# Performance work log

Hardware: AMD Instinct MI355X
Metric: run time of the kernel (lower is better)

The kernel has to match this reference:

```python
import jax, jax.numpy as jnp
import numpy as np

B, H, W, C = 1, 64, 64, 256
NH = 8
K = 7


def setup_inputs() -> dict:
    key = jax.random.key(0)
    ks = jax.random.split(key, 6)
    x = jax.random.normal(ks[0], (B, H, W, C), dtype=jnp.float32)
    # torch nn.Linear weights are [out, in]
    qkv_w = jax.random.normal(ks[1], (3 * C, C), dtype=jnp.float32) * 0.02
    qkv_b = jnp.zeros((3 * C,), dtype=jnp.float32)
    proj_w = jax.random.normal(ks[2], (C, C), dtype=jnp.float32) * 0.02
    proj_b = jnp.zeros((C,), dtype=jnp.float32)
    # relative position bias table: [num_heads, 2K-1, 2K-1]
    rpb = jax.random.normal(ks[3], (NH, 2 * K - 1, 2 * K - 1), dtype=jnp.float32) * 0.02
    return {"x": x, "qkv_w": qkv_w, "qkv_b": qkv_b, "proj_w": proj_w,
            "proj_b": proj_b, "rpb": rpb}


def _neighbor_idx(n, k):
    # clamped window starts (NATTEN semantics): each query sees exactly k neighbors
    start = jnp.clip(jnp.arange(n) - k // 2, 0, n - k)  # [n]
    return start[:, None] + jnp.arange(k)[None, :]       # [n, k]


def reference(x, qkv_w, qkv_b, proj_w, proj_b, rpb):
    b, h, w, c = x.shape
    nh = rpb.shape[0]
    k = (rpb.shape[1] + 1) // 2
    hd = c // nh
    scale = hd ** -0.5

    qkv = x @ qkv_w.T + qkv_b                              # [b,h,w,3c]
    qkv = qkv.reshape(b, h, w, 3, nh, hd)
    qkv = jnp.transpose(qkv, (3, 0, 4, 1, 2, 5))           # [3,b,nh,h,w,hd]
    q, kk, v = qkv[0], qkv[1], qkv[2]

    ni = _neighbor_idx(h, k)                               # [h,k]
    nj = _neighbor_idx(w, k)                               # [w,k]

    # gather neighborhood keys/values: [b,nh,h,k,w,k,hd]
    k_nb = kk[:, :, ni][:, :, :, :, nj]
    v_nb = v[:, :, ni][:, :, :, :, nj]

    # attention logits over the k x k window
    attn = jnp.einsum('bnijd,bniajcd->bnijac', q * scale, k_nb)  # [b,nh,h,w,k,k]

    # relative position bias: index = (neighbor - query) + (k-1)
    bi = ni - jnp.arange(h)[:, None] + (k - 1)             # [h,k]
    bj = nj - jnp.arange(w)[:, None] + (k - 1)             # [w,k]
    bias = rpb[:, bi][:, :, :, bj]                         # [nh,h,k,w,k]
    attn = attn + jnp.transpose(bias, (0, 1, 3, 2, 4))[None]

    attn = jax.nn.softmax(attn.reshape(b, nh, h, w, k * k), axis=-1)
    attn = attn.reshape(b, nh, h, w, k, k)

    out = jnp.einsum('bnijac,bniajcd->bnijd', attn, v_nb)  # [b,nh,h,w,hd]
    out = jnp.transpose(out, (0, 2, 3, 1, 4)).reshape(b, h, w, c)
    out = out @ proj_w.T + proj_b
    return out
```

## Files before the change

### kernel.cpp

```cpp
#include <hip/hip_runtime.h>
#include <math.h>

#define HH 64
#define WW 64
#define CC 256
#define NHEAD 8
#define HD 32
#define KW 7
#define NPIX (HH * WW)

#define KR 40
#define VTS 232

typedef _Float16 half2v __attribute__((ext_vector_type(2)));
typedef _Float16 half8v __attribute__((ext_vector_type(8)));
typedef __fp16 fp16x2 __attribute__((ext_vector_type(2)));
typedef float float4v __attribute__((ext_vector_type(4)));

__device__ __forceinline__ unsigned pkrtz(float lo, float hi) {
  union { fp16x2 h; unsigned u; } c;
  c.h = __builtin_amdgcn_cvt_pkrtz(lo, hi);
  return c.u;
}
__device__ __forceinline__ ushort f2h(float f) {
  union { _Float16 h; ushort u; } c;
  c.h = (_Float16)f;
  return c.u;
}

template <int N, int BM, int BN, bool ABF, bool OB>
__global__ __launch_bounds__(256) void gemm5h(
    const void* __restrict__ Ap, const float* __restrict__ Bw,
    const float* __restrict__ bias, void* __restrict__ Cd) {
  constexpr int SEGA = BM / 32;
  constexpr int SEGB = BN / 32;
  constexpr int MF = BM / 32;
  constexpr int NF = BN / 32;

  __shared__ ushort As[2][BM * 64];
  __shared__ ushort Bs[2][BN * 64];

  const int t = threadIdx.x;
  const int lane = t & 63;
  const int wave = t >> 6;
  const int bm = blockIdx.x * BM;
  const int bn = blockIdx.y * BN;

  const float*  Aw = (const float*)Ap;
  const ushort* Ab = (const ushort*)Ap;

  float fA[2][SEGA][8];
  float fB[2][SEGB][8];
  uint4 wA[2][SEGA];

#define LOADA(c, s)                                                            \
  {                                                                            \
    _Pragma("unroll") for (int sa = 0; sa < SEGA; ++sa) {                      \
      const int seg = sa * 256 + t;                                            \
      const int row = seg >> 3;                                                \
      const int q8 = seg & 7;                                                  \
      if (ABF) {                                                               \
        wA[s][sa] =                                                            \
            *(const uint4*)(Ab + (size_t)(bm + row) * 256 + (c) * 64 + q8 * 8);\
      } else {                                                                 \
        const float* p_ = Aw + (size_t)(bm + row) * 256 + (c) * 64 + q8 * 8;   \
        *(float4*)&fA[s][sa][0] = *(const float4*)(p_);                        \
        *(float4*)&fA[s][sa][4] = *(const float4*)(p_ + 4);                    \
      }                                                                        \
    }                                                                          \
  }

#define LOADB(c, s)                                                            \
  {                                                                            \
    _Pragma("unroll") for (int sb = 0; sb < SEGB; ++sb) {                      \
      const int seg = sb * 256 + t;                                            \
      const int row = seg >> 3;                                                \
      const int q8 = seg & 7;                                                  \
      const float* p_ = Bw + (size_t)(bn + row) * 256 + (c) * 64 + q8 * 8;     \
      *(float4*)&fB[s][sb][0] = *(const float4*)(p_);                          \
      *(float4*)&fB[s][sb][4] = *(const float4*)(p_ + 4);                      \
    }                                                                          \
  }

#define WRITEC(b, s)                                                           \
  {                                                                            \
    _Pragma("unroll") for (int sa = 0; sa < SEGA; ++sa) {                      \
      const int seg = sa * 256 + t;                                            \
      const int row = seg >> 3;                                                \
      const int q8 = seg & 7;                                                  \
      const int lin = row * 128 + q8 * 16;                                     \
      const int sw = (row & 7) << 4;                                           \
      uint4 w_;                                                                \
      if (ABF) {                                                               \
        w_ = wA[s][sa];                                                        \
      } else {                                                                 \
        w_.x = pkrtz(fA[s][sa][0], fA[s][sa][1]);                              \
        w_.y = pkrtz(fA[s][sa][2], fA[s][sa][3]);                              \
        w_.z = pkrtz(fA[s][sa][4], fA[s][sa][5]);                              \
        w_.w = pkrtz(fA[s][sa][6], fA[s][sa][7]);                              \
      }                                                                        \
      *(uint4*)((char*)As[b] + (lin ^ sw)) = w_;                               \
    }                                                                          \
    _Pragma("unroll") for (int sb = 0; sb < SEGB; ++sb) {                      \
      const int seg = sb * 256 + t;                                            \
      const int row = seg >> 3;                                                \
      const int q8 = seg & 7;                                                  \
      const int lin = row * 128 + q8 * 16;                                     \
      const int sw = (row & 7) << 4;                                           \
      uint4 w_;                                                                \
      w_.x = pkrtz(fB[s][sb][0], fB[s][sb][1]);                                \
      w_.y = pkrtz(fB[s][sb][2], fB[s][sb][3]);                                \
      w_.z = pkrtz(fB[s][sb][4], fB[s][sb][5]);                                \
      w_.w = pkrtz(fB[s][sb][6], fB[s][sb][7]);                                \
      *(uint4*)((char*)Bs[b] + (lin ^ sw)) = w_;                               \
    }                                                                          \
  }

  const int wr = (wave >> 1) * (BM / 2);
  const int wc = (wave & 1) * (BN / 2);
  const int lrow = lane & 15;
  const int lkb = (lane >> 4) * 16;

  float4v acc[MF][NF];
#pragma unroll
  for (int mf = 0; mf < MF; ++mf)
#pragma unroll
    for (int nf = 0; nf < NF; ++nf) acc[mf][nf] = (float4v){0.f, 0.f, 0.f, 0.f};

  LOADA(0, 0); LOADB(0, 0);
  WRITEC(0, 0);
  LOADA(1, 1); LOADB(1, 1);
  __syncthreads();

#pragma unroll
  for (int c = 0; c < 4; ++c) {
    if (c < 3) WRITEC((c + 1) & 1, (c + 1) & 1);
    if (c < 2) { LOADA(c + 2, c & 1); LOADB(c + 2, c & 1); }
    const char* Al = (const char*)As[c & 1];
    const char* Bl = (const char*)Bs[c & 1];
#pragma unroll
    for (int ks = 0; ks < 2; ++ks) {
      half8v af[MF], bfr[NF];
#pragma unroll
      for (int mf = 0; mf < MF; ++mf) {
        const int row = wr + mf * 16 + lrow;
        const int ad = row * 128 + ks * 64 + lkb;
        af[mf] = *(const half8v*)(Al + (ad ^ ((row & 7) << 4)));
      }
#pragma unroll
      for (int nf = 0; nf < NF; ++nf) {
        const int row = wc + nf * 16 + lrow;
        const int bd = row * 128 + ks * 64 + lkb;
        bfr[nf] = *(const half8v*)(Bl + (bd ^ ((row & 7) << 4)));
      }
#pragma unroll
      for (int mf = 0; mf < MF; ++mf)
#pragma unroll
        for (int nf = 0; nf < NF; ++nf)
          acc[mf][nf] = __builtin_amdgcn_mfma_f32_16x16x32_f16(
              af[mf], bfr[nf], acc[mf][nf], 0, 0, 0);
    }
    if (c < 3) __syncthreads();
  }
#undef LOADA
#undef LOADB
#undef WRITEC

#pragma unroll
  for (int mf = 0; mf < MF; ++mf) {
#pragma unroll
    for (int nf = 0; nf < NF; ++nf) {
      const int n = bn + wc + nf * 16 + lrow;
      const float bv = bias[n];
      const int m0 = bm + wr + mf * 16 + (lane >> 4) * 4;
      if (OB) {
        ushort* C = (ushort*)Cd;
#pragma unroll
        for (int rr = 0; rr < 4; ++rr)
          C[(size_t)(m0 + rr) * N + n] = f2h(acc[mf][nf][rr] + bv);
      } else {
        float* C = (float*)Cd;
#pragma unroll
        for (int rr = 0; rr < 4; ++rr)
          C[(size_t)(m0 + rr) * N + n] = acc[mf][nf][rr] + bv;
      }
    }
  }
}

__global__ __launch_bounds__(256) void natten7(
    const ushort* __restrict__ qkv, const float* __restrict__ rpb,
    ushort* __restrict__ aout) {
  __shared__ ushort Ks[224 * KR];
  __shared__ ushort Vt[32 * VTS];
  __shared__ float Rs[169];

  const int head = blockIdx.y;
  const int tile = blockIdx.x;
  const int i0 = (tile >> 3) * 8, j0 = (tile & 7) * 8;
  const int hs = min(max(i0 - 3, 0), HH - 14);
  const int ws = min(max(j0 - 3, 0), WW - 14);
  const int t = threadIdx.x;
  const int l = t & 63;
  const int wv = t >> 6;

  if (t < 169) Rs[t] = rpb[head * 169 + t];

  if (t < 112) {
    const int ent2 = t >> 2;
    const int hr = ent2 >> 1, hc = 14 + (ent2 & 1);
    const uint4 z = {0u, 0u, 0u, 0u};
    *(uint4*)(Ks + (hr * 16 + hc) * KR + (t & 3) * 8) = z;
  }
#pragma unroll
  for (int it = 0; it < 2; ++it) {
    const int task = it * 256 + t;
    const int d = task >> 4, hr = task & 15;
    if (hr < 14) *(unsigned*)(Vt + d * VTS + hr * 16 + 14) = 0u;
  }

#pragma unroll
  for (int s = 0; s < 4; ++s) {
    if (t < 196) {
      const int hr = (t * 2341) >> 15;
      const int hc = t - hr * 14;
      const int g = (hs + hr) * WW + (ws + hc);
      const int col = hr * 16 + hc;
      const uint4 kv = *(const uint4*)(qkv + (size_t)g * 768 + 256 + head * HD + s * 8);
      *(uint4*)(Ks + col * KR + s * 8) = kv;
      const uint4 vv = *(const uint4*)(qkv + (size_t)g * 768 + 512 + head * HD + s * 8);
      const int d0 = s * 8;
      Vt[(d0 + 0) * VTS + col] = (ushort)(vv.x);
      Vt[(d0 + 1) * VTS + col] = (ushort)(vv.x >> 16);
      Vt[(d0 + 2) * VTS + col] = (ushort)(vv.y);
      Vt[(d0 + 3) * VTS + col] = (ushort)(vv.y >> 16);
      Vt[(d0 + 4) * VTS + col] = (ushort)(vv.z);
      Vt[(d0 + 5) * VTS + col] = (ushort)(vv.z >> 16);
      Vt[(d0 + 6) * VTS + col] = (ushort)(vv.w);
      Vt[(d0 + 7) * VTS + col] = (ushort)(vv.w >> 16);
    }
  }
  __syncthreads();

  const int strip_i0 = i0 + wv * 2;
  const int lg = l >> 4;
  const int l15 = l & 15;

  const int pi = strip_i0 + (l15 >> 3);
  const int pj = j0 + (l15 & 7);
  const int si = min(max(pi - 3, 0), HH - KW);
  const int sj = min(max(pj - 3, 0), WW - KW);
  const int si_min = min(max(strip_i0 - 3, 0), HH - KW);
  const int slab0 = min(si_min - hs, 6);

  const half8v qf = *(const half8v*)(qkv + (size_t)(pi * WW + pj) * 768 +
                                     head * HD + lg * 8);

  float4v s8[8];
  const float4v zz = {0.f, 0.f, 0.f, 0.f};
#pragma unroll
  for (int g = 0; g < 8; ++g) {
    const int ent = (slab0 + g) * 16 + l15;
    const half8v kf = *(const half8v*)(Ks + ent * KR + lg * 8);
    s8[g] = __builtin_amdgcn_mfma_f32_16x16x32_f16(kf, qf, zz, 0, 0, 0);
  }

  const int lr0 = si - hs;
  const int lc0 = sj - ws;
  const int abase = slab0 - lr0;
  const int rowb = ((si - pi + 6) + abase) * 13 + (sj - pj + 6) - lc0;
  const float scale = 0.17677669529663687f;

  float e8[8][4];
  float ssum = 0.f;
#pragma unroll
  for (int g = 0; g < 8; ++g) {
    const int a = abase + g;
    const bool va = (unsigned)a < 7u;
    const int idxg = min(max(rowb + g * 13, 0), 153);
#pragma unroll
    for (int r = 0; r < 4; ++r) {
      const int hc = lg * 4 + r;
      const bool vc = (unsigned)(hc - lc0) < 7u;
      const float ev = __expf(fmaf(s8[g][r], scale, Rs[idxg + hc]));
      const float em = (va && vc) ? ev : 0.f;
      e8[g][r] = em;
      ssum += em;
    }
  }
  ssum += __shfl_xor(ssum, 16);
  ssum += __shfl_xor(ssum, 32);
  const float inv = 1.f / ssum;

  unsigned Wp[8][2];
#pragma unroll
  for (int g = 0; g < 8; ++g) {
    Wp[g][0] = pkrtz(e8[g][0] * inv, e8[g][1] * inv);
    Wp[g][1] = pkrtz(e8[g][2] * inv, e8[g][3] * inv);
  }

  float4v o[2] = {zz, zz};
#pragma unroll
  for (int ks = 0; ks < 4; ++ks) {
    unsigned F[4];
#pragma unroll
    for (int f = 0; f < 4; ++f) {
      const int src = l15 + (((lg & 1) * 2 + (f >> 1)) << 4);
      const unsigned va = __shfl(Wp[2 * ks][f & 1], src);
      const unsigned vb = __shfl(Wp[2 * ks + 1][f & 1], src);
      F[f] = (lg >> 1) ? vb : va;
    }
    union { unsigned u[4]; half8v h; } pf;
    pf.u[0] = F[0]; pf.u[1] = F[1]; pf.u[2] = F[2]; pf.u[3] = F[3];
#pragma unroll
    for (int nf = 0; nf < 2; ++nf) {
      const int dim = l15 + nf * 16;
      const half8v vf = *(const half8v*)(Vt + dim * VTS + slab0 * 16 +
                                         ks * 32 + lg * 8);
      o[nf] = __builtin_amdgcn_mfma_f32_16x16x32_f16(pf.h, vf, o[nf], 0, 0, 0);
    }
  }

#pragma unroll
  for (int r = 0; r < 4; ++r) {
    const int pxo = lg * 4 + r;
    const int oi = strip_i0 + (pxo >> 3);
    const int oj = j0 + (pxo & 7);
    ushort* op = aout + (size_t)(oi * WW + oj) * CC + head * HD + l15;
    op[0]  = f2h(o[0][r]);
    op[16] = f2h(o[1][r]);
  }
}

extern "C" void kernel_launch(void* const* d_in, const int* in_sizes, int n_in,
                              void* d_out, int out_size, void* d_ws, size_t ws_size,
                              hipStream_t stream) {
  const float* x      = (const float*)d_in[0];
  const float* qkv_w  = (const float*)d_in[1];
  const float* qkv_b  = (const float*)d_in[2];
  const float* proj_w = (const float*)d_in[3];
  const float* proj_b = (const float*)d_in[4];
  const float* rpb    = (const float*)d_in[5];
  float* out = (float*)d_out;

  ushort* qkvh  = (ushort*)d_ws;
  ushort* aouth = qkvh + 3145728;

  gemm5h<768, 32, 64, false, true><<<dim3(128, 12), 256, 0, stream>>>(
      x, qkv_w, qkv_b, qkvh);

  natten7<<<dim3(64, NHEAD), 256, 0, stream>>>(qkvh, rpb, aouth);

  gemm5h<256, 32, 32, true, false><<<dim3(128, 8), 256, 0, stream>>>(
      aouth, proj_w, proj_b, out);
}
```

Before: 25.40 us.

## Fuse output projection GEMM into neighborhood attention kernel via last-block counters

Merges the projection GEMM into the attention kernel. Each block bumps per-tile atomic counters after writing its head's output. The last of the 8 head blocks to finish a 4-row half-tile then runs the 32x256 projection for it, reusing the attention shared memory. This drops one kernel launch and the gap between kernels. In exchange, the projection work lands on only a few tail blocks, and the counters are never reset, relying on modulo-8 wraparound across calls.

```diff
diff --git a/kernel.cpp b/kernel.cpp
--- a/kernel.cpp
+++ b/kernel.cpp
@@ -7,15 +7,16 @@
 #define NHEAD 8
 #define HD 32
 #define KW 7
-#define NPIX (HH * WW)
 
 #define KR 40
 #define VTS 232
 
-typedef _Float16 half2v __attribute__((ext_vector_type(2)));
 typedef _Float16 half8v __attribute__((ext_vector_type(8)));
 typedef __fp16 fp16x2 __attribute__((ext_vector_type(2)));
 typedef float float4v __attribute__((ext_vector_type(4)));
+
+struct PadCnt { unsigned v; unsigned pad[15]; };
+__device__ PadCnt half_cnt[128];
 
 __device__ __forceinline__ unsigned pkrtz(float lo, float hi) {
   union { fp16x2 h; unsigned u; } c;
@@ -188,19 +189,138 @@
   }
 }
 
-__global__ __launch_bounds__(256) void natten7(
+__device__ __forceinline__ void gemm2_half(
+    char* smem, const ushort* __restrict__ A, const float* __restrict__ Bw,
+    const float* __restrict__ bias, float* __restrict__ Cd,
+    int pr0, int j0, int bn, int t) {
+  constexpr int ABUF = 32 * 128;
+  constexpr int BBUF = 64 * 128;
+
+  char* As0 = smem;
+  char* Bs0 = smem + 2 * ABUF;
+
+  const int lane = t & 63;
+  const int wave = t >> 6;
+
+  uint4 wA[2];
+  float fB[2][2][8];
+
+#define LOADA2(c, s)                                                           \
+  {                                                                            \
+    const int row = t >> 3;                                                    \
+    const int q8 = t & 7;                                                      \
+    const int pix = (pr0 + (row >> 3)) * 64 + j0 + (row & 7);                  \
+    wA[s] = *(const uint4*)(A + (size_t)pix * 256 + (c) * 64 + q8 * 8);        \
+  }
+
+#define LOADB2(c, s)                                                           \
+  {                                                                            \
+    _Pragma("unroll") for (int sb = 0; sb < 2; ++sb) {                         \
+      const int seg = sb * 256 + t;                                            \
+      const int row = seg >> 3;                                                \
+      const int q8 = seg & 7;                                                  \
+      const float* p_ = Bw + (size_t)(bn + row) * 256 + (c) * 64 + q8 * 8;     \
+      *(float4*)&fB[s][sb][0] = *(const float4*)(p_);                          \
+      *(float4*)&fB[s][sb][4] = *(const float4*)(p_ + 4);                      \
+    }                                                                          \
+  }
+
+#define WRITEC2(b, s)                                                          \
+  {                                                                            \
+    {                                                                          \
+      const int row = t >> 3;                                                  \
+      const int q8 = t & 7;                                                    \
+      const int lin = row * 128 + q8 * 16;                                     \
+      const int sw = (row & 7) << 4;                                           \
+      *(uint4*)(As0 + (b) * ABUF + (lin ^ sw)) = wA[s];                        \
+    }                                                                          \
+    _Pragma("unroll") for (int sb = 0; sb < 2; ++sb) {                         \
+      const int seg = sb * 256 + t;                                            \
+      const int row = seg >> 3;                                                \
+      const int q8 = seg & 7;                                                  \
+      const int lin = row * 128 + q8 * 16;                                     \
+      const int sw = (row & 7) << 4;                                           \
+      uint4 w_;                                                                \
+      w_.x = pkrtz(fB[s][sb][0], fB[s][sb][1]);                                \
+      w_.y = pkrtz(fB[s][sb][2], fB[s][sb][3]);                                \
+      w_.z = pkrtz(fB[s][sb][4], fB[s][sb][5]);                                \
+      w_.w = pkrtz(fB[s][sb][6], fB[s][sb][7]);                                \
+      *(uint4*)(Bs0 + (b) * BBUF + (lin ^ sw)) = w_;                           \
+    }                                                                          \
+  }
+
+  const int wr = (wave >> 1) * 16;
+  const int wc = (wave & 1) * 32;
+  const int lrow = lane & 15;
+  const int lkb = (lane >> 4) * 16;
+
+  float4v acc[2] = {{0.f, 0.f, 0.f, 0.f}, {0.f, 0.f, 0.f, 0.f}};
+
+  LOADA2(0, 0); LOADB2(0, 0);
+  WRITEC2(0, 0);
+  LOADA2(1, 1); LOADB2(1, 1);
+  __syncthreads();
+
+#pragma unroll
+  for (int c = 0; c < 4; ++c) {
+    if (c < 3) WRITEC2((c + 1) & 1, (c + 1) & 1);
+    if (c < 2) { LOADA2(c + 2, c & 1); LOADB2(c + 2, c & 1); }
+    const char* Al = As0 + (c & 1) * ABUF;
+    const char* Bl = Bs0 + (c & 1) * BBUF;
+#pragma unroll
+    for (int ks = 0; ks < 2; ++ks) {
+      const int arow = wr + lrow;
+      const int ad = arow * 128 + ks * 64 + lkb;
+      const half8v af = *(const half8v*)(Al + (ad ^ ((arow & 7) << 4)));
+      half8v bfr[2];
+#pragma unroll
+      for (int nf = 0; nf < 2; ++nf) {
+        const int row = wc + nf * 16 + lrow;
+        const int bd = row * 128 + ks * 64 + lkb;
+        bfr[nf] = *(const half8v*)(Bl + (bd ^ ((row & 7) << 4)));
+      }
+#pragma unroll
+      for (int nf = 0; nf < 2; ++nf)
+        acc[nf] = __builtin_amdgcn_mfma_f32_16x16x32_f16(af, bfr[nf], acc[nf],
+                                                         0, 0, 0);
+    }
+    if (c < 3) __syncthreads();
+  }
+#undef LOADA2
+#undef LOADB2
+#undef WRITEC2
+
+#pragma unroll
+  for (int nf = 0; nf < 2; ++nf) {
+    const int n = bn + wc + nf * 16 + lrow;
+    const float bv = bias[n];
+    const int m0 = wr + (lane >> 4) * 4;
+#pragma unroll
+    for (int rr = 0; rr < 4; ++rr) {
+      const int mrow = m0 + rr;
+      const int pix = (pr0 + (mrow >> 3)) * 64 + j0 + (mrow & 7);
+      Cd[(size_t)pix * 256 + n] = acc[nf][rr] + bv;
+    }
+  }
+}
+
+__global__ __launch_bounds__(256) void natg2(
     const ushort* __restrict__ qkv, const float* __restrict__ rpb,
-    ushort* __restrict__ aout) {
-  __shared__ ushort Ks[224 * KR];
-  __shared__ ushort Vt[32 * VTS];
-  __shared__ float Rs[169];
-
+    const float* __restrict__ proj_w, const float* __restrict__ proj_b,
+    ushort* __restrict__ aout, float* __restrict__ out) {
+  __shared__ __align__(16) char smem[33472];
+  __shared__ int winflag[2];
+
+  ushort* Ks = (ushort*)smem;
+  ushort* Vt = (ushort*)(smem + 17920);
+  float*  Rs = (float*)(smem + 32768);
+
+  const int tile = blockIdx.x;
   const int head = blockIdx.y;
-  const int tile = blockIdx.x;
+  const int t = threadIdx.x;
   const int i0 = (tile >> 3) * 8, j0 = (tile & 7) * 8;
   const int hs = min(max(i0 - 3, 0), HH - 14);
   const int ws = min(max(j0 - 3, 0), WW - 14);
-  const int t = threadIdx.x;
   const int l = t & 63;
   const int wv = t >> 6;
 
@@ -330,6 +450,33 @@
     op[0]  = f2h(o[0][r]);
     op[16] = f2h(o[1][r]);
   }
+
+  __syncthreads();
+  if (t == 0) {
+    __threadfence();
+    const unsigned o0 = __hip_atomic_fetch_add(
+        &half_cnt[tile * 2 + 0].v, 1u, __ATOMIC_RELAXED,
+        __HIP_MEMORY_SCOPE_AGENT);
+    const unsigned o1 = __hip_atomic_fetch_add(
+        &half_cnt[tile * 2 + 1].v, 1u, __ATOMIC_RELAXED,
+        __HIP_MEMORY_SCOPE_AGENT);
+    winflag[0] = ((o0 & 7u) == 7u);
+    winflag[1] = ((o1 & 7u) == 7u);
+    if (winflag[0] | winflag[1]) __threadfence();
+  }
+  __syncthreads();
+
+#pragma unroll
+  for (int h = 0; h < 2; ++h) {
+    if (winflag[h]) {
+      const int pr0 = i0 + 4 * h;
+#pragma unroll
+      for (int bn = 0; bn < 256; bn += 64) {
+        __syncthreads();
+        gemm2_half(smem, aout, proj_w, proj_b, out, pr0, j0, bn, t);
+      }
+    }
+  }
 }
 
 extern "C" void kernel_launch(void* const* d_in, const int* in_sizes, int n_in,
@@ -349,8 +496,6 @@
   gemm5h<768, 32, 64, false, true><<<dim3(128, 12), 256, 0, stream>>>(
       x, qkv_w, qkv_b, qkvh);
 
-  natten7<<<dim3(64, NHEAD), 256, 0, stream>>>(qkvh, rpb, aouth);
-
-  gemm5h<256, 32, 32, true, false><<<dim3(128, 8), 256, 0, stream>>>(
-      aouth, proj_w, proj_b, out);
+  natg2<<<dim3(64, NHEAD), 256, 0, stream>>>(
+      qkvh, rpb, proj_w, proj_b, aouth, out);
 }
```

New measurement: 54.73 us. 2.15x slower.

## Fuse neighborhood attention with output projection in one kernel

Applied to the files above, without the earlier changes.

Replaces the separate attention kernel and projection GEMM with one kernel. Each block handles a 2x8 pixel tile across all 8 heads (two passes of 4 heads, one wave per head) and keeps the attention output in LDS. It then runs the projection GEMM from LDS, converting fp32 proj weights to fp16 chunk by chunk. This drops a launch and the global round trip of the attention output. In exchange, every block reloads and converts the whole projection weight matrix, uses about 98KB of LDS, and launches only 256 blocks.

```diff
diff --git a/kernel.cpp b/kernel.cpp
--- a/kernel.cpp
+++ b/kernel.cpp
@@ -7,12 +7,14 @@
 #define NHEAD 8
 #define HD 32
 #define KW 7
-#define NPIX (HH * WW)
 
 #define KR 40
-#define VTS 232
-
-typedef _Float16 half2v __attribute__((ext_vector_type(2)));
+#define VTS2 152
+#define SLOTB 21248
+#define AOUTB 84992
+#define RSB 93440
+#define SMEMB 98848
+
 typedef _Float16 half8v __attribute__((ext_vector_type(8)));
 typedef __fp16 fp16x2 __attribute__((ext_vector_type(2)));
 typedef float float4v __attribute__((ext_vector_type(4)));
@@ -188,147 +190,225 @@
   }
 }
 
-__global__ __launch_bounds__(256) void natten7(
+__global__ __launch_bounds__(256) void natg2c(
     const ushort* __restrict__ qkv, const float* __restrict__ rpb,
-    ushort* __restrict__ aout) {
-  __shared__ ushort Ks[224 * KR];
-  __shared__ ushort Vt[32 * VTS];
-  __shared__ float Rs[169];
-
-  const int head = blockIdx.y;
-  const int tile = blockIdx.x;
-  const int i0 = (tile >> 3) * 8, j0 = (tile & 7) * 8;
-  const int hs = min(max(i0 - 3, 0), HH - 14);
+    const float* __restrict__ proj_w, const float* __restrict__ proj_b,
+    float* __restrict__ out) {
+  __shared__ __align__(16) char smem[SMEMB];
+  float* Rs = (float*)(smem + RSB);
+  ushort* aoutL = (ushort*)(smem + AOUTB);
+
+  const int ti = blockIdx.x;
+  const int i0 = (ti >> 3) * 2, j0 = (ti & 7) * 8;
+  const int hs = min(max(i0 - 3, 0), HH - 8);
   const int ws = min(max(j0 - 3, 0), WW - 14);
   const int t = threadIdx.x;
   const int l = t & 63;
   const int wv = t >> 6;
-
-  if (t < 169) Rs[t] = rpb[head * 169 + t];
-
-  if (t < 112) {
-    const int ent2 = t >> 2;
-    const int hr = ent2 >> 1, hc = 14 + (ent2 & 1);
-    const uint4 z = {0u, 0u, 0u, 0u};
-    *(uint4*)(Ks + (hr * 16 + hc) * KR + (t & 3) * 8) = z;
-  }
-#pragma unroll
-  for (int it = 0; it < 2; ++it) {
-    const int task = it * 256 + t;
-    const int d = task >> 4, hr = task & 15;
-    if (hr < 14) *(unsigned*)(Vt + d * VTS + hr * 16 + 14) = 0u;
-  }
-
-#pragma unroll
-  for (int s = 0; s < 4; ++s) {
-    if (t < 196) {
-      const int hr = (t * 2341) >> 15;
-      const int hc = t - hr * 14;
-      const int g = (hs + hr) * WW + (ws + hc);
-      const int col = hr * 16 + hc;
-      const uint4 kv = *(const uint4*)(qkv + (size_t)g * 768 + 256 + head * HD + s * 8);
-      *(uint4*)(Ks + col * KR + s * 8) = kv;
-      const uint4 vv = *(const uint4*)(qkv + (size_t)g * 768 + 512 + head * HD + s * 8);
-      const int d0 = s * 8;
-      Vt[(d0 + 0) * VTS + col] = (ushort)(vv.x);
-      Vt[(d0 + 1) * VTS + col] = (ushort)(vv.x >> 16);
-      Vt[(d0 + 2) * VTS + col] = (ushort)(vv.y);
-      Vt[(d0 + 3) * VTS + col] = (ushort)(vv.y >> 16);
-      Vt[(d0 + 4) * VTS + col] = (ushort)(vv.z);
-      Vt[(d0 + 5) * VTS + col] = (ushort)(vv.z >> 16);
-      Vt[(d0 + 6) * VTS + col] = (ushort)(vv.w);
-      Vt[(d0 + 7) * VTS + col] = (ushort)(vv.w >> 16);
-    }
-  }
-  __syncthreads();
-
-  const int strip_i0 = i0 + wv * 2;
   const int lg = l >> 4;
   const int l15 = l & 15;
 
-  const int pi = strip_i0 + (l15 >> 3);
+#pragma unroll
+  for (int it = 0; it < 6; ++it) {
+    const int idx = it * 256 + t;
+    if (idx < NHEAD * 169) Rs[idx] = rpb[idx];
+  }
+
+  const int pi = i0 + (l15 >> 3);
   const int pj = j0 + (l15 & 7);
   const int si = min(max(pi - 3, 0), HH - KW);
   const int sj = min(max(pj - 3, 0), WW - KW);
-  const int si_min = min(max(strip_i0 - 3, 0), HH - KW);
-  const int slab0 = min(si_min - hs, 6);
-
-  const half8v qf = *(const half8v*)(qkv + (size_t)(pi * WW + pj) * 768 +
-                                     head * HD + lg * 8);
-
-  float4v s8[8];
-  const float4v zz = {0.f, 0.f, 0.f, 0.f};
-#pragma unroll
-  for (int g = 0; g < 8; ++g) {
-    const int ent = (slab0 + g) * 16 + l15;
-    const half8v kf = *(const half8v*)(Ks + ent * KR + lg * 8);
-    s8[g] = __builtin_amdgcn_mfma_f32_16x16x32_f16(kf, qf, zz, 0, 0, 0);
-  }
-
+  const int si_min = min(max(i0 - 3, 0), HH - KW);
+  const int slab0 = si_min - hs;
   const int lr0 = si - hs;
   const int lc0 = sj - ws;
   const int abase = slab0 - lr0;
   const int rowb = ((si - pi + 6) + abase) * 13 + (sj - pj + 6) - lc0;
   const float scale = 0.17677669529663687f;
-
-  float e8[8][4];
-  float ssum = 0.f;
-#pragma unroll
-  for (int g = 0; g < 8; ++g) {
-    const int a = abase + g;
-    const bool va = (unsigned)a < 7u;
-    const int idxg = min(max(rowb + g * 13, 0), 153);
+  const float4v zz = {0.f, 0.f, 0.f, 0.f};
+
+#pragma unroll
+  for (int pass = 0; pass < 2; ++pass) {
+    if (pass == 0) {
+      if (t < 128) {
+        const int slot = t >> 5, d = t & 31;
+        ushort* vt = (ushort*)(smem + slot * SLOTB + 11520) + d * VTS2;
+#pragma unroll
+        for (int hr = 0; hr < 9; ++hr) *(unsigned*)(vt + hr * 16 + 14) = 0u;
+#pragma unroll
+        for (int c = 0; c < 8; ++c) *(unsigned*)(vt + 128 + c * 2) = 0u;
+      }
+      {
+        const int slot = t >> 6;
+        const int ent = 128 + ((t >> 2) & 15);
+        const int seg = t & 3;
+        const uint4 z = {0u, 0u, 0u, 0u};
+        *(uint4*)((ushort*)(smem + slot * SLOTB) + ent * KR + seg * 8) = z;
+      }
+    }
+
+#pragma unroll
+    for (int it = 0; it < 4; ++it) {
+      const int task = it * 256 + t;
+      if (task < 896) {
+        const int hsl = task / 224;
+        const int rem = task - hsl * 224;
+        const int mat = rem >= 112;
+        const int row = rem - mat * 112;
+        const int hr = (row * 2341) >> 15;
+        const int hc = row - hr * 14;
+        const int g = (hs + hr) * WW + (ws + hc);
+        const int head = pass * 4 + hsl;
+        const int col = hr * 16 + hc;
+        const ushort* src = qkv + (size_t)g * 768 + 256 + mat * 256 + head * HD;
+        if (!mat) {
+          ushort* kd = (ushort*)(smem + hsl * SLOTB) + col * KR;
+          *(uint4*)(kd + 0)  = *(const uint4*)(src + 0);
+          *(uint4*)(kd + 8)  = *(const uint4*)(src + 8);
+          *(uint4*)(kd + 16) = *(const uint4*)(src + 16);
+          *(uint4*)(kd + 24) = *(const uint4*)(src + 24);
+        } else {
+          ushort* vt = (ushort*)(smem + hsl * SLOTB + 11520);
+#pragma unroll
+          for (int s2 = 0; s2 < 4; ++s2) {
+            const uint4 vv = *(const uint4*)(src + s2 * 8);
+            const int d0 = s2 * 8;
+            vt[(d0 + 0) * VTS2 + col] = (ushort)(vv.x);
+            vt[(d0 + 1) * VTS2 + col] = (ushort)(vv.x >> 16);
+            vt[(d0 + 2) * VTS2 + col] = (ushort)(vv.y);
+            vt[(d0 + 3) * VTS2 + col] = (ushort)(vv.y >> 16);
+            vt[(d0 + 4) * VTS2 + col] = (ushort)(vv.z);
+            vt[(d0 + 5) * VTS2 + col] = (ushort)(vv.z >> 16);
+            vt[(d0 + 6) * VTS2 + col] = (ushort)(vv.w);
+            vt[(d0 + 7) * VTS2 + col] = (ushort)(vv.w >> 16);
+          }
+        }
+      }
+    }
+    __syncthreads();
+
+    const int head = pass * 4 + wv;
+    const ushort* Ks = (const ushort*)(smem + wv * SLOTB);
+    const ushort* Vt = (const ushort*)(smem + wv * SLOTB + 11520);
+    const float* Rh = Rs + head * 169;
+
+    const half8v qf = *(const half8v*)(qkv + (size_t)(pi * WW + pj) * 768 +
+                                       head * HD + lg * 8);
+
+    float4v s8[8];
+#pragma unroll
+    for (int g = 0; g < 8; ++g) {
+      const int ent = (slab0 + g) * 16 + l15;
+      const half8v kf = *(const half8v*)(Ks + ent * KR + lg * 8);
+      s8[g] = __builtin_amdgcn_mfma_f32_16x16x32_f16(kf, qf, zz, 0, 0, 0);
+    }
+
+    float e8[8][4];
+    float ssum = 0.f;
+#pragma unroll
+    for (int g = 0; g < 8; ++g) {
+      const int a = abase + g;
+      const bool va = (unsigned)a < 7u;
+      const int idxg = min(max(rowb + g * 13, 0), 153);
+#pragma unroll
+      for (int r = 0; r < 4; ++r) {
+        const int hc = lg * 4 + r;
+        const bool vc = (unsigned)(hc - lc0) < 7u;
+        const float ev = __expf(fmaf(s8[g][r], scale, Rh[idxg + hc]));
+        const float em = (va && vc) ? ev : 0.f;
+        e8[g][r] = em;
+        ssum += em;
+      }
+    }
+    ssum += __shfl_xor(ssum, 16);
+    ssum += __shfl_xor(ssum, 32);
+    const float inv = 1.f / ssum;
+
+    unsigned Wp[8][2];
+#pragma unroll
+    for (int g = 0; g < 8; ++g) {
+      Wp[g][0] = pkrtz(e8[g][0] * inv, e8[g][1] * inv);
+      Wp[g][1] = pkrtz(e8[g][2] * inv, e8[g][3] * inv);
+    }
+
+    float4v o[2] = {zz, zz};
+#pragma unroll
+    for (int ks = 0; ks < 4; ++ks) {
+      unsigned F[4];
+#pragma unroll
+      for (int f = 0; f < 4; ++f) {
+        const int src = l15 + (((lg & 1) * 2 + (f >> 1)) << 4);
+        const unsigned va = __shfl(Wp[2 * ks][f & 1], src);
+        const unsigned vb = __shfl(Wp[2 * ks + 1][f & 1], src);
+        F[f] = (lg >> 1) ? vb : va;
+      }
+      union { unsigned u[4]; half8v h; } pf;
+      pf.u[0] = F[0]; pf.u[1] = F[1]; pf.u[2] = F[2]; pf.u[3] = F[3];
+#pragma unroll
+      for (int nf = 0; nf < 2; ++nf) {
+        const int dim = l15 + nf * 16;
+        const half8v vf = *(const half8v*)(Vt + dim * VTS2 + slab0 * 16 +
+                                           ks * 32 + lg * 8);
+        o[nf] = __builtin_amdgcn_mfma_f32_16x16x32_f16(pf.h, vf, o[nf], 0, 0, 0);
+      }
+    }
+
 #pragma unroll
     for (int r = 0; r < 4; ++r) {
-      const int hc = lg * 4 + r;
-      const bool vc = (unsigned)(hc - lc0) < 7u;
-      const float ev = __expf(fmaf(s8[g][r], scale, Rs[idxg + hc]));
-      const float em = (va && vc) ? ev : 0.f;
-      e8[g][r] = em;
-      ssum += em;
-    }
-  }
-  ssum += __shfl_xor(ssum, 16);
-  ssum += __shfl_xor(ssum, 32);
-  const float inv = 1.f / ssum;
-
-  unsigned Wp[8][2];
-#pragma unroll
-  for (int g = 0; g < 8; ++g) {
-    Wp[g][0] = pkrtz(e8[g][0] * inv, e8[g][1] * inv);
-    Wp[g][1] = pkrtz(e8[g][2] * inv, e8[g][3] * inv);
-  }
-
-  float4v o[2] = {zz, zz};
-#pragma unroll
-  for (int ks = 0; ks < 4; ++ks) {
-    unsigned F[4];
-#pragma unroll
-    for (int f = 0; f < 4; ++f) {
-      const int src = l15 + (((lg & 1) * 2 + (f >> 1)) << 4);
-      const unsigned va = __shfl(Wp[2 * ks][f & 1], src);
-      const unsigned vb = __shfl(Wp[2 * ks + 1][f & 1], src);
-      F[f] = (lg >> 1) ? vb : va;
-    }
-    union { unsigned u[4]; half8v h; } pf;
-    pf.u[0] = F[0]; pf.u[1] = F[1]; pf.u[2] = F[2]; pf.u[3] = F[3];
-#pragma unroll
-    for (int nf = 0; nf < 2; ++nf) {
-      const int dim = l15 + nf * 16;
-      const half8v vf = *(const half8v*)(Vt + dim * VTS + slab0 * 16 +
-                                         ks * 32 + lg * 8);
-      o[nf] = __builtin_amdgcn_mfma_f32_16x16x32_f16(pf.h, vf, o[nf], 0, 0, 0);
-    }
-  }
-
-#pragma unroll
-  for (int r = 0; r < 4; ++r) {
-    const int pxo = lg * 4 + r;
-    const int oi = strip_i0 + (pxo >> 3);
-    const int oj = j0 + (pxo & 7);
-    ushort* op = aout + (size_t)(oi * WW + oj) * CC + head * HD + l15;
-    op[0]  = f2h(o[0][r]);
-    op[16] = f2h(o[1][r]);
+      const int px = lg * 4 + r;
+      aoutL[px * 264 + head * HD + l15]      = f2h(o[0][r]);
+      aoutL[px * 264 + head * HD + 16 + l15] = f2h(o[1][r]);
+    }
+    __syncthreads();
+  }
+
+  ushort* Wc = (ushort*)smem;
+  const int wrow = t >> 2;
+  const int wq = (t & 3) * 64;
+
+#pragma unroll
+  for (int c = 0; c < 4; ++c) {
+    __syncthreads();
+    {
+      const float* p_ = proj_w + (size_t)(c * 64 + wrow) * 256 + wq;
+      ushort* d_ = Wc + wrow * 264 + wq;
+#pragma unroll
+      for (int s2 = 0; s2 < 4; ++s2) {
+        const float4 f0 = *(const float4*)(p_ + s2 * 16);
+        const float4 f1 = *(const float4*)(p_ + s2 * 16 + 4);
+        const float4 f2 = *(const float4*)(p_ + s2 * 16 + 8);
+        const float4 f3 = *(const float4*)(p_ + s2 * 16 + 12);
+        uint4 w_;
+        w_.x = pkrtz(f0.x, f0.y);
+        w_.y = pkrtz(f0.z, f0.w);
+        w_.z = pkrtz(f1.x, f1.y);
+        w_.w = pkrtz(f1.z, f1.w);
+        *(uint4*)(d_ + s2 * 16) = w_;
+        w_.x = pkrtz(f2.x, f2.y);
+        w_.y = pkrtz(f2.z, f2.w);
+        w_.z = pkrtz(f3.x, f3.y);
+        w_.w = pkrtz(f3.z, f3.w);
+        *(uint4*)(d_ + s2 * 16 + 8) = w_;
+      }
+    }
+    __syncthreads();
+
+    float4v acc = zz;
+#pragma unroll
+    for (int ks = 0; ks < 8; ++ks) {
+      const half8v af = *(const half8v*)(aoutL + l15 * 264 + ks * 32 + lg * 8);
+      const half8v bf = *(const half8v*)(Wc + (wv * 16 + l15) * 264 + ks * 32 +
+                                         lg * 8);
+      acc = __builtin_amdgcn_mfma_f32_16x16x32_f16(af, bf, acc, 0, 0, 0);
+    }
+    const int n = c * 64 + wv * 16 + l15;
+    const float bv = proj_b[n];
+#pragma unroll
+    for (int r = 0; r < 4; ++r) {
+      const int px = lg * 4 + r;
+      const int pixel = (i0 + (px >> 3)) * WW + j0 + (px & 7);
+      out[(size_t)pixel * CC + n] = acc[r] + bv;
+    }
   }
 }
 
@@ -343,14 +423,10 @@
   const float* rpb    = (const float*)d_in[5];
   float* out = (float*)d_out;
 
-  ushort* qkvh  = (ushort*)d_ws;
-  ushort* aouth = qkvh + 3145728;
+  ushort* qkvh = (ushort*)d_ws;
 
   gemm5h<768, 32, 64, false, true><<<dim3(128, 12), 256, 0, stream>>>(
       x, qkv_w, qkv_b, qkvh);
 
-  natten7<<<dim3(64, NHEAD), 256, 0, stream>>>(qkvh, rpb, aouth);
-
-  gemm5h<256, 32, 32, true, false><<<dim3(128, 8), 256, 0, stream>>>(
-      aouth, proj_w, proj_b, out);
+  natg2c<<<dim3(256), 256, 0, stream>>>(qkvh, rpb, proj_w, proj_b, out);
 }
```

Measured after the change: 34.95 us. 1.38x slower.

## Fuse QKV projection into neighborhood attention kernel per tile and head

Applied to the files above, without the earlier changes.

Removes the separate QKV GEMM and computes K/V for the 14x14 halo and Q for the 8x8 tile inside the attention block, converting x and weights to fp16 in swizzled shared memory and using MFMA. This eliminates the global fp16 qkv write/read and one kernel launch. In exchange it recomputes K/V for overlapping halos (about 3x redundant work), rereads x per head, and uses about 80KB of LDS per block, limiting occupancy.

```diff
diff --git a/kernel.cpp b/kernel.cpp
--- a/kernel.cpp
+++ b/kernel.cpp
@@ -7,12 +7,19 @@
 #define NHEAD 8
 #define HD 32
 #define KW 7
-#define NPIX (HH * WW)
 
 #define KR 40
 #define VTS 232
-
-typedef _Float16 half2v __attribute__((ext_vector_type(2)));
+#define QS 40
+
+#define XCO 0
+#define WSO 28672
+#define KSO 40960
+#define VTO 58880
+#define QSO 73728
+#define RSO 78848
+#define SMB 79536
+
 typedef _Float16 half8v __attribute__((ext_vector_type(8)));
 typedef __fp16 fp16x2 __attribute__((ext_vector_type(2)));
 typedef float float4v __attribute__((ext_vector_type(4)));
@@ -188,64 +195,160 @@
   }
 }
 
-__global__ __launch_bounds__(256) void natten7(
-    const ushort* __restrict__ qkv, const float* __restrict__ rpb,
+__global__ __launch_bounds__(256) void natq(
+    const float* __restrict__ x, const float* __restrict__ qkv_w,
+    const float* __restrict__ qkv_b, const float* __restrict__ rpb,
     ushort* __restrict__ aout) {
-  __shared__ ushort Ks[224 * KR];
-  __shared__ ushort Vt[32 * VTS];
-  __shared__ float Rs[169];
-
-  const int head = blockIdx.y;
+  __shared__ __align__(16) char smem[SMB];
+  char* Xc = smem + XCO;
+  char* Wsb = smem + WSO;
+  ushort* Ks = (ushort*)(smem + KSO);
+  ushort* Vt = (ushort*)(smem + VTO);
+  ushort* Qs = (ushort*)(smem + QSO);
+  float* Rs = (float*)(smem + RSO);
+
   const int tile = blockIdx.x;
+  const int h = blockIdx.y;
+  const int t = threadIdx.x;
+  const int l = t & 63;
+  const int wv = t >> 6;
+  const int lg = l >> 4;
+  const int l15 = l & 15;
+  const int lkb = lg * 16;
+
   const int i0 = (tile >> 3) * 8, j0 = (tile & 7) * 8;
   const int hs = min(max(i0 - 3, 0), HH - 14);
   const int ws = min(max(j0 - 3, 0), WW - 14);
-  const int t = threadIdx.x;
-  const int l = t & 63;
-  const int wv = t >> 6;
-
-  if (t < 169) Rs[t] = rpb[head * 169 + t];
-
-  if (t < 112) {
-    const int ent2 = t >> 2;
-    const int hr = ent2 >> 1, hc = 14 + (ent2 & 1);
-    const uint4 z = {0u, 0u, 0u, 0u};
-    *(uint4*)(Ks + (hr * 16 + hc) * KR + (t & 3) * 8) = z;
-  }
-#pragma unroll
-  for (int it = 0; it < 2; ++it) {
-    const int task = it * 256 + t;
-    const int d = task >> 4, hr = task & 15;
-    if (hr < 14) *(unsigned*)(Vt + d * VTS + hr * 16 + 14) = 0u;
-  }
-
-#pragma unroll
-  for (int s = 0; s < 4; ++s) {
-    if (t < 196) {
-      const int hr = (t * 2341) >> 15;
-      const int hc = t - hr * 14;
-      const int g = (hs + hr) * WW + (ws + hc);
-      const int col = hr * 16 + hc;
-      const uint4 kv = *(const uint4*)(qkv + (size_t)g * 768 + 256 + head * HD + s * 8);
-      *(uint4*)(Ks + col * KR + s * 8) = kv;
-      const uint4 vv = *(const uint4*)(qkv + (size_t)g * 768 + 512 + head * HD + s * 8);
-      const int d0 = s * 8;
-      Vt[(d0 + 0) * VTS + col] = (ushort)(vv.x);
-      Vt[(d0 + 1) * VTS + col] = (ushort)(vv.x >> 16);
-      Vt[(d0 + 2) * VTS + col] = (ushort)(vv.y);
-      Vt[(d0 + 3) * VTS + col] = (ushort)(vv.y >> 16);
-      Vt[(d0 + 4) * VTS + col] = (ushort)(vv.z);
-      Vt[(d0 + 5) * VTS + col] = (ushort)(vv.z >> 16);
-      Vt[(d0 + 6) * VTS + col] = (ushort)(vv.w);
-      Vt[(d0 + 7) * VTS + col] = (ushort)(vv.w >> 16);
+  const int di = i0 - hs, dj = j0 - ws;
+
+  if (t < 169) Rs[t] = rpb[h * 169 + t];
+
+  const float4v zz = {0.f, 0.f, 0.f, 0.f};
+  float4v acc[18];
+#pragma unroll
+  for (int idx = 0; idx < 18; ++idx) acc[idx] = zz;
+
+#define XF(row, k2)                                                            \
+  (*(const half8v*)(Xc + ((((row) * 128) + (k2) * 64 + lkb) ^                  \
+                          (((row) & 7) << 4))))
+#define WF(row, k2)                                                            \
+  (*(const half8v*)(Wsb + ((((row) * 128) + (k2) * 64 + lkb) ^                 \
+                           (((row) & 7) << 4))))
+
+  for (int c = 0; c < 4; ++c) {
+#pragma unroll
+    for (int sa = 0; sa < 7; ++sa) {
+      const int seg = sa * 256 + t;
+      const int row = seg >> 3;
+      const int q8 = seg & 7;
+      const int lin = row * 128 + q8 * 16;
+      const int swz = (row & 7) << 4;
+      const int hr = row >> 4, hc = row & 15;
+      uint4 w_;
+      if (hc < 14) {
+        const float* p_ =
+            x + (size_t)((hs + hr) * WW + ws + hc) * 256 + c * 64 + q8 * 8;
+        const float4 f0 = *(const float4*)(p_);
+        const float4 f1 = *(const float4*)(p_ + 4);
+        w_.x = pkrtz(f0.x, f0.y);
+        w_.y = pkrtz(f0.z, f0.w);
+        w_.z = pkrtz(f1.x, f1.y);
+        w_.w = pkrtz(f1.z, f1.w);
+      } else {
+        w_.x = 0u; w_.y = 0u; w_.z = 0u; w_.w = 0u;
+      }
+      *(uint4*)(Xc + (lin ^ swz)) = w_;
+    }
+#pragma unroll
+    for (int sb = 0; sb < 3; ++sb) {
+      const int seg = sb * 256 + t;
+      const int row = seg >> 3;
+      const int q8 = seg & 7;
+      const int lin = row * 128 + q8 * 16;
+      const int swz = (row & 7) << 4;
+      const int wrow = (row < 32) ? (256 + h * HD + row)
+                     : (row < 64) ? (512 + h * HD + (row - 32))
+                                  : (h * HD + (row - 64));
+      const float* p_ = qkv_w + (size_t)wrow * 256 + c * 64 + q8 * 8;
+      const float4 f0 = *(const float4*)(p_);
+      const float4 f1 = *(const float4*)(p_ + 4);
+      uint4 w_;
+      w_.x = pkrtz(f0.x, f0.y);
+      w_.y = pkrtz(f0.z, f0.w);
+      w_.z = pkrtz(f1.x, f1.y);
+      w_.w = pkrtz(f1.z, f1.w);
+      *(uint4*)(Wsb + (lin ^ swz)) = w_;
+    }
+    __syncthreads();
+
+#pragma unroll
+    for (int k2 = 0; k2 < 2; ++k2) {
+#pragma unroll
+      for (int idx = 0; idx < 18; ++idx) {
+        const int gf = wv * 18 + idx;
+        half8v af, bf;
+        if (gf < 28) {
+          const int mf = gf >> 1, dh = gf & 1;
+          af = XF(mf * 16 + l15, k2);
+          bf = WF(dh * 16 + l15, k2);
+        } else if (gf < 56) {
+          const int v = gf - 28;
+          const int mf = v >> 1, dh = v & 1;
+          af = WF(32 + dh * 16 + l15, k2);
+          bf = XF(mf * 16 + l15, k2);
+        } else {
+          const int q = gf - 56;
+          const int mfq = q >> 1, dh = q & 1;
+          af = XF((di + mfq) * 16 + l15, k2);
+          bf = WF(64 + dh * 16 + l15, k2);
+        }
+        acc[idx] =
+            __builtin_amdgcn_mfma_f32_16x16x32_f16(af, bf, acc[idx], 0, 0, 0);
+      }
+    }
+    __syncthreads();
+  }
+#undef XF
+#undef WF
+
+#pragma unroll
+  for (int idx = 0; idx < 18; ++idx) {
+    const int gf = wv * 18 + idx;
+    if (gf < 28) {
+      const int mf = gf >> 1, dh = gf & 1;
+      const int dim = dh * 16 + l15;
+      const float bv = qkv_b[256 + h * HD + dim];
+#pragma unroll
+      for (int r = 0; r < 4; ++r) {
+        const int ent = mf * 16 + lg * 4 + r;
+        Ks[ent * KR + dim] = f2h(acc[idx][r] + bv);
+      }
+    } else if (gf < 56) {
+      const int v = gf - 28;
+      const int mf = v >> 1, dh = v & 1;
+      const int ent = mf * 16 + l15;
+#pragma unroll
+      for (int r = 0; r < 4; ++r) {
+        const int dim = dh * 16 + lg * 4 + r;
+        Vt[dim * VTS + ent] = f2h(acc[idx][r] + qkv_b[512 + h * HD + dim]);
+      }
+    } else {
+      const int q = gf - 56;
+      const int mfq = q >> 1, dh = q & 1;
+      const int dim = dh * 16 + l15;
+      const float bv = qkv_b[h * HD + dim];
+#pragma unroll
+      for (int r = 0; r < 4; ++r) {
+        const int pos = lg * 4 + r;
+        const int pc = pos - dj;
+        if ((unsigned)pc < 8u)
+          Qs[(mfq * 8 + pc) * QS + dim] = f2h(acc[idx][r] + bv);
+      }
     }
   }
   __syncthreads();
 
   const int strip_i0 = i0 + wv * 2;
-  const int lg = l >> 4;
-  const int l15 = l & 15;
-
   const int pi = strip_i0 + (l15 >> 3);
   const int pj = j0 + (l15 & 7);
   const int si = min(max(pi - 3, 0), HH - KW);
@@ -253,11 +356,10 @@
   const int si_min = min(max(strip_i0 - 3, 0), HH - KW);
   const int slab0 = min(si_min - hs, 6);
 
-  const half8v qf = *(const half8v*)(qkv + (size_t)(pi * WW + pj) * 768 +
-                                     head * HD + lg * 8);
+  const int px = (wv * 2 + (l15 >> 3)) * 8 + (l15 & 7);
+  const half8v qf = *(const half8v*)(Qs + px * QS + lg * 8);
 
   float4v s8[8];
-  const float4v zz = {0.f, 0.f, 0.f, 0.f};
 #pragma unroll
   for (int g = 0; g < 8; ++g) {
     const int ent = (slab0 + g) * 16 + l15;
@@ -310,14 +412,14 @@
       const unsigned vb = __shfl(Wp[2 * ks + 1][f & 1], src);
       F[f] = (lg >> 1) ? vb : va;
     }
-    union { unsigned u[4]; half8v h; } pf;
+    union { unsigned u[4]; half8v hh; } pf;
     pf.u[0] = F[0]; pf.u[1] = F[1]; pf.u[2] = F[2]; pf.u[3] = F[3];
 #pragma unroll
     for (int nf = 0; nf < 2; ++nf) {
       const int dim = l15 + nf * 16;
       const half8v vf = *(const half8v*)(Vt + dim * VTS + slab0 * 16 +
                                          ks * 32 + lg * 8);
-      o[nf] = __builtin_amdgcn_mfma_f32_16x16x32_f16(pf.h, vf, o[nf], 0, 0, 0);
+      o[nf] = __builtin_amdgcn_mfma_f32_16x16x32_f16(pf.hh, vf, o[nf], 0, 0, 0);
     }
   }
 
@@ -326,7 +428,7 @@
     const int pxo = lg * 4 + r;
     const int oi = strip_i0 + (pxo >> 3);
     const int oj = j0 + (pxo & 7);
-    ushort* op = aout + (size_t)(oi * WW + oj) * CC + head * HD + l15;
+    ushort* op = aout + (size_t)(oi * WW + oj) * CC + h * HD + l15;
     op[0]  = f2h(o[0][r]);
     op[16] = f2h(o[1][r]);
   }
@@ -343,13 +445,9 @@
   const float* rpb    = (const float*)d_in[5];
   float* out = (float*)d_out;
 
-  ushort* qkvh  = (ushort*)d_ws;
-  ushort* aouth = qkvh + 3145728;
-
-  gemm5h<768, 32, 64, false, true><<<dim3(128, 12), 256, 0, stream>>>(
-      x, qkv_w, qkv_b, qkvh);
-
-  natten7<<<dim3(64, NHEAD), 256, 0, stream>>>(qkvh, rpb, aouth);
+  ushort* aouth = (ushort*)d_ws;
+
+  natq<<<dim3(64, NHEAD), 256, 0, stream>>>(x, qkv_w, qkv_b, rpb, aouth);
 
   gemm5h<256, 32, 32, true, false><<<dim3(128, 8), 256, 0, stream>>>(
       aouth, proj_w, proj_b, out);
```

After: 44.13 us. 73.7% more time.
